# Optimization experiments

Measured on AMD Instinct MI355X. Metric: run time of the kernel, lower is better.

The kernel has to match this reference:

```python
import jax, jax.numpy as jnp
import numpy as np

D = 1024
H = 16
FF = 4 * D


def layer_norm(x, g, b, eps=1e-5):
    mu = jnp.mean(x, axis=-1, keepdims=True)
    var = jnp.var(x, axis=-1, keepdims=True)
    return (x - mu) * jax.lax.rsqrt(var + eps) * g + b


def setup_inputs() -> dict:
    key = jax.random.key(0)
    ks = jax.random.split(key, 8)
    s = lambda fan_in: 1.0 / np.sqrt(fan_in)
    return {
        "x": jax.random.normal(ks[0], (2, 2048, D), dtype=jnp.float32),
        "ln1_g": jnp.ones((D,), jnp.float32),
        "ln1_b": jnp.zeros((D,), jnp.float32),
        "w_qkv": jax.random.uniform(ks[1], (D, 3 * D), jnp.float32, -s(D), s(D)),
        "b_qkv": jnp.zeros((3 * D,), jnp.float32),
        "w_out": jax.random.uniform(ks[2], (D, D), jnp.float32, -s(D), s(D)),
        "b_out": jnp.zeros((D,), jnp.float32),
        "ln2_g": jnp.ones((D,), jnp.float32),
        "ln2_b": jnp.zeros((D,), jnp.float32),
        "w_fc1": jax.random.uniform(ks[3], (D, FF), jnp.float32, -s(D), s(D)),
        "b_fc1": jnp.zeros((FF,), jnp.float32),
        "w_fc2": jax.random.uniform(ks[4], (FF, D), jnp.float32, -s(FF), s(FF)),
        "b_fc2": jnp.zeros((D,), jnp.float32),
    }


def reference(x, ln1_g, ln1_b, w_qkv, b_qkv, w_out, b_out,
              ln2_g, ln2_b, w_fc1, b_fc1, w_fc2, b_fc2):
    b, n, c = x.shape
    hd = c // H
    scale = hd ** -0.5

    # --- pre-norm MHA ---
    h = layer_norm(x, ln1_g, ln1_b)
    qkv = h @ w_qkv + b_qkv                      # [b,n,3c]
    qkv = qkv.reshape(b, n, 3, H, hd)
    q = jnp.transpose(qkv[:, :, 0], (0, 2, 1, 3))  # [b,H,n,hd]
    k = jnp.transpose(qkv[:, :, 1], (0, 2, 1, 3))
    v = jnp.transpose(qkv[:, :, 2], (0, 2, 1, 3))
    attn = jnp.einsum('bhqd,bhkd->bhqk', q, k) * scale
    attn = jax.nn.softmax(attn, axis=-1)
    o = jnp.einsum('bhqk,bhkd->bhqd', attn, v)   # [b,H,n,hd]
    o = jnp.transpose(o, (0, 2, 1, 3)).reshape(b, n, c)
    x = x + (o @ w_out + b_out)

    # --- pre-norm FFN ---
    h = layer_norm(x, ln2_g, ln2_b)
    h = jax.nn.gelu(h @ w_fc1 + b_fc1, approximate=False)
    x = x + (h @ w_fc2 + b_fc2)
    return x
```

## Files before the change

kernel.cpp:

```cpp
#include <hip/hip_runtime.h>
#include <stdint.h>
#include <math.h>

#define D_MODEL 1024
#define NHEAD   16
#define HDIM    64
#define FFDIM   4096
#define SEQ     2048
#define BATCH   2
#define NTOK    (BATCH*SEQ)
#define QKVN    (3*D_MODEL)

typedef __bf16 bf16;
typedef __attribute__((ext_vector_type(8))) __bf16 bf16x8;
typedef __attribute__((ext_vector_type(4))) __bf16 bf16x4;
typedef __attribute__((ext_vector_type(4))) float f32x4;

__device__ __forceinline__ void gld_lds16(const void* g, void* l) {
    __builtin_amdgcn_global_load_lds((__attribute__((address_space(1))) void*)g,
                                     (__attribute__((address_space(3))) void*)l,
                                     16, 0, 0);
}

__device__ __forceinline__ float fast_exp2(float x) {
#if __has_builtin(__builtin_amdgcn_exp2f)
    return __builtin_amdgcn_exp2f(x);
#else
    return __expf(x * 0.69314718056f);
#endif
}

__device__ __forceinline__ float fast_rcp(float x) {
#if __has_builtin(__builtin_amdgcn_rcpf)
    return __builtin_amdgcn_rcpf(x);
#else
    return 1.0f / x;
#endif
}

__device__ __forceinline__ float gelu_fast(float x) {
    float xx = x * x;
    float y  = x * fmaf(0.035677408137f, xx, 0.7978845608f);
    float z  = fminf(-2.8853900817779268f * y, 126.0f);
    float e  = fast_exp2(z);
    return x * fast_rcp(1.0f + e);
}

#define BARRIER() do {                                         \
    __builtin_amdgcn_s_barrier();                              \
    asm volatile("" ::: "memory");                             \
} while (0)
#define LGKM0() asm volatile("s_waitcnt lgkmcnt(0)" ::: "memory")
#define VMW(N)  asm volatile("s_waitcnt vmcnt(" #N ")" ::: "memory")

#define PHASE_BAR() do {                                       \
    asm volatile("s_waitcnt vmcnt(0)" ::: "memory");           \
    __builtin_amdgcn_s_barrier();                              \
    asm volatile("" ::: "memory");                             \
} while (0)

#define GEMM_BAR() do {                                        \
    asm volatile("s_waitcnt lgkmcnt(0)" ::: "memory");         \
    __builtin_amdgcn_s_barrier();                              \
    asm volatile("" ::: "memory");                             \
} while (0)

__global__ __launch_bounds__(256)
void k_transpose_all(const float* __restrict__ w_qkv, const float* __restrict__ w_out,
                     const float* __restrict__ w_fc1, const float* __restrict__ w_fc2,
                     bf16* __restrict__ t_qkv, bf16* __restrict__ t_out,
                     bf16* __restrict__ t_fc1, bf16* __restrict__ t_fc2) {
    __shared__ float tile[32][33];
    int bid = blockIdx.x;
    const float* W; bf16* Wt; int K, N, ti;
    if (bid < 3072)       { W = w_qkv; Wt = t_qkv; K = 1024; N = 3072; ti = bid; }
    else if (bid < 4096)  { W = w_out; Wt = t_out; K = 1024; N = 1024; ti = bid - 3072; }
    else if (bid < 8192)  { W = w_fc1; Wt = t_fc1; K = 1024; N = 4096; ti = bid - 4096; }
    else                  { W = w_fc2; Wt = t_fc2; K = 4096; N = 1024; ti = bid - 8192; }
    int tn = N >> 5;
    int n0 = (ti % tn) * 32, k0 = (ti / tn) * 32;
    int tx = threadIdx.x, ty = threadIdx.y;
#pragma unroll
    for (int i = 0; i < 4; i++)
        tile[ty + i * 8][tx] = W[(size_t)(k0 + ty + i * 8) * N + n0 + tx];
    __syncthreads();
#pragma unroll
    for (int i = 0; i < 4; i++)
        Wt[(size_t)(n0 + ty + i * 8) * K + k0 + tx] = (bf16)tile[tx][ty + i * 8];
}

__global__ __launch_bounds__(256)
void k_vtrans(const bf16* __restrict__ qkv, bf16* __restrict__ vT) {
    __shared__ bf16 t[32][33];
    int tok0 = blockIdx.x * 32, f0 = blockIdx.y * 32;
    int tx = threadIdx.x, ty = threadIdx.y;
#pragma unroll
    for (int i = 0; i < 4; i++)
        t[ty + i * 8][tx] = qkv[(size_t)(tok0 + ty + i * 8) * QKVN + 2 * D_MODEL + f0 + tx];
    __syncthreads();
    int s = tx;
    int pp = (s < 16) ? ((s >> 2) * 8 + (s & 3))
                      : (((s - 16) >> 2) * 8 + ((s - 16) & 3) + 4);
#pragma unroll
    for (int i = 0; i < 4; i++)
        vT[(size_t)(f0 + ty + i * 8) * NTOK + tok0 + pp] = t[tx][ty + i * 8];
}

__global__ __launch_bounds__(256)
void k_layernorm(const float* __restrict__ x, const float* __restrict__ g,
                 const float* __restrict__ b, bf16* __restrict__ out) {
    int row = blockIdx.x;
    int tid = threadIdx.x;
    float4 v = ((const float4*)(x + (size_t)row * D_MODEL))[tid];
    float s  = v.x + v.y + v.z + v.w;
    float ss = v.x * v.x + v.y * v.y + v.z * v.z + v.w * v.w;
#pragma unroll
    for (int off = 32; off > 0; off >>= 1) {
        s  += __shfl_down(s, off, 64);
        ss += __shfl_down(ss, off, 64);
    }
    __shared__ float red[2][4];
    __shared__ float mv[2];
    int wave = tid >> 6, lane = tid & 63;
    if (lane == 0) { red[0][wave] = s; red[1][wave] = ss; }
    __syncthreads();
    if (tid == 0) {
        float S  = red[0][0] + red[0][1] + red[0][2] + red[0][3];
        float SS = red[1][0] + red[1][1] + red[1][2] + red[1][3];
        float mu = S * (1.0f / D_MODEL);
        float var = SS * (1.0f / D_MODEL) - mu * mu;
        mv[0] = mu;
        mv[1] = rsqrtf(var + 1e-5f);
    }
    __syncthreads();
    float mu = mv[0], rs = mv[1];
    float4 gv = ((const float4*)g)[tid];
    float4 bv = ((const float4*)b)[tid];
    bf16x4 ov = { (bf16)((v.x - mu) * rs * gv.x + bv.x),
                  (bf16)((v.y - mu) * rs * gv.y + bv.y),
                  (bf16)((v.z - mu) * rs * gv.z + bv.z),
                  (bf16)((v.w - mu) * rs * gv.w + bv.w) };
    *(bf16x4*)(out + (size_t)row * D_MODEL + tid * 4) = ov;
}

template <int DO_GELU, int ATOMIC, int SPLITK>
__global__ __launch_bounds__(512, 2)
void k_gemm256(const bf16* __restrict__ A, const bf16* __restrict__ Bt,
               const float* __restrict__ bias, bf16* __restrict__ outb,
               float* __restrict__ outf, int M, int N, int K) {
    __shared__ bf16 LA[2][2][8192];
    __shared__ bf16 LB[2][2][8192];

    int tid = threadIdx.x;
    int wid = tid >> 6, lane = tid & 63;
    int quad = lane >> 4, l16 = lane & 15;
    int wm = (wid >> 2) * 128;
    int wn = (wid & 3) * 64;

    int nwg = gridDim.x * gridDim.y;
    int bid = blockIdx.y * gridDim.x + blockIdx.x;
    int sid = (bid & 7) * (nwg >> 3) + (bid >> 3);
    int bx = sid % gridDim.x, by = sid / gridDim.x;
    int m0 = by * 256, n0 = bx * 256;

    int Keff = (SPLITK > 1) ? (K / SPLITK) : K;
    int koff = (SPLITK > 1) ? blockIdx.z * Keff : 0;

    int l = lane;
    int rsw = l >> 2;
    int csw = 8 * ((l & 3) ^ ((l >> 3) & 3));
    const bf16* pA = A  + (size_t)(m0 + 32 * wid + rsw) * K + koff + csw;
    const bf16* pB = Bt + (size_t)(n0 + 32 * wid + rsw) * K + koff + csw;
    int sbase = wid * 1024;

    int xq = 8 * (quad ^ ((l16 >> 1) & 3));

    f32x4 acc[8][4];
#pragma unroll
    for (int i = 0; i < 8; i++)
#pragma unroll
        for (int j = 0; j < 4; j++) acc[i][j] = (f32x4){0.f, 0.f, 0.f, 0.f};

#define STAGE_A(buf, kh, t) do {                                               \
    gld_lds16(pA + (size_t)(t) * 64 + (kh) * 32,              &LA[buf][kh][sbase]);       \
    gld_lds16(pA + (size_t)16 * K + (size_t)(t) * 64 + (kh) * 32, &LA[buf][kh][sbase + 512]); \
} while (0)
#define STAGE_B(buf, kh, t) do {                                               \
    gld_lds16(pB + (size_t)(t) * 64 + (kh) * 32,              &LB[buf][kh][sbase]);       \
    gld_lds16(pB + (size_t)16 * K + (size_t)(t) * 64 + (kh) * 32, &LB[buf][kh][sbase + 512]); \
} while (0)

    bf16x8 af[4], bfr[4];
#define RD_B(buf, kh)  do {                                                    \
    _Pragma("unroll")                                                          \
    for (int fc = 0; fc < 4; fc++)                                             \
        bfr[fc] = *(const bf16x8*)&LB[buf][kh][(wn + fc * 16 + l16) * 32 + xq];\
} while (0)
#define RD_A(buf, kh, rh) do {                                                 \
    _Pragma("unroll")                                                          \
    for (int fr = 0; fr < 4; fr++)                                             \
        af[fr] = *(const bf16x8*)&LA[buf][kh][(wm + (rh) * 64 + fr * 16 + l16) * 32 + xq]; \
} while (0)
#define MFMA16(rh) do {                                                        \
    __builtin_amdgcn_s_setprio(1);                                             \
    _Pragma("unroll")                                                          \
    for (int fr = 0; fr < 4; fr++)                                             \
        _Pragma("unroll")                                                      \
        for (int fc = 0; fc < 4; fc++)                                         \
            acc[(rh) * 4 + fr][fc] =                                           \
                __builtin_amdgcn_mfma_f32_16x16x32_bf16(af[fr], bfr[fc],       \
                                                        acc[(rh) * 4 + fr][fc], 0, 0, 0); \
    __builtin_amdgcn_s_setprio(0);                                             \
} while (0)

    int nt = Keff / 64;
    int buf = 0;
    STAGE_A(0, 0, 0); STAGE_B(0, 0, 0);
    STAGE_A(0, 1, 0); STAGE_B(0, 1, 0);
    VMW(4); BARRIER();

    for (int t = 0; t < nt - 1; t++) {
        RD_B(buf, 0); RD_A(buf, 0, 0);
        STAGE_A(buf ^ 1, 0, t + 1);
        BARRIER(); LGKM0();
        MFMA16(0);
        BARRIER();
        RD_A(buf, 0, 1);
        STAGE_B(buf ^ 1, 0, t + 1);
        BARRIER(); LGKM0();
        MFMA16(1);
        VMW(4); BARRIER();
        RD_B(buf, 1); RD_A(buf, 1, 0);
        STAGE_A(buf ^ 1, 1, t + 1);
        BARRIER(); LGKM0();
        MFMA16(0);
        BARRIER();
        RD_A(buf, 1, 1);
        STAGE_B(buf ^ 1, 1, t + 1);
        BARRIER(); LGKM0();
        MFMA16(1);
        VMW(4); BARRIER();
        buf ^= 1;
    }
    RD_B(buf, 0); RD_A(buf, 0, 0);
    BARRIER(); LGKM0();
    MFMA16(0);
    BARRIER();
    RD_A(buf, 0, 1);
    BARRIER(); LGKM0();
    MFMA16(1);
    VMW(0); BARRIER();
    RD_B(buf, 1); RD_A(buf, 1, 0);
    BARRIER(); LGKM0();
    MFMA16(0);
    BARRIER();
    RD_A(buf, 1, 1);
    LGKM0();
    MFMA16(1);

#undef STAGE_A
#undef STAGE_B
#undef RD_A
#undef RD_B
#undef MFMA16

#pragma unroll
    for (int fi = 0; fi < 8; fi++) {
        int row = m0 + wm + fi * 16 + quad * 4;
#pragma unroll
        for (int fc = 0; fc < 4; fc++) {
            int col = n0 + wn + fc * 16 + l16;
            if constexpr (ATOMIC) {
                float bb = (SPLITK == 1 || blockIdx.z == 0) ? bias[col] : 0.0f;
#pragma unroll
                for (int r = 0; r < 4; r++)
                    atomicAdd(&outf[(size_t)(row + r) * N + col], acc[fi][fc][r] + bb);
            } else {
                float bb = bias[col];
#pragma unroll
                for (int r = 0; r < 4; r++) {
                    float v = acc[fi][fc][r] + bb;
                    if (DO_GELU) v = gelu_fast(v);
                    outb[(size_t)(row + r) * N + col] = (bf16)v;
                }
            }
        }
    }
}

template <int DO_GELU, int DO_RES, int OUT_BF16, int BN>
__global__ __launch_bounds__(256)
void k_gemm(const bf16* __restrict__ A, const bf16* __restrict__ Bt,
            const float* __restrict__ bias, const float* __restrict__ res,
            float* __restrict__ outf, bf16* __restrict__ outb,
            int M, int N, int K) {
    constexpr int WN = BN / 32;
    __shared__ bf16 As[2][128 * 32];
    __shared__ bf16 Bs[2][BN * 32];
    int tid  = threadIdx.x;
    int wave = tid >> 6, lane = tid & 63;
    int quad = lane >> 4, l16 = lane & 15;

    int nwg = gridDim.x * gridDim.y;
    int bid = blockIdx.y * gridDim.x + blockIdx.x;
    int sid = (bid & 7) * (nwg >> 3) + (bid >> 3);
    int bx = sid % gridDim.x, by = sid / gridDim.x;
    int m0 = by * 128, n0 = bx * BN;
    int wm = (wave >> 1) * 64, wn = (wave & 1) * (BN / 2);

    f32x4 acc[4][WN];
#pragma unroll
    for (int i = 0; i < 4; i++)
#pragma unroll
        for (int j = 0; j < WN; j++) acc[i][j] = (f32x4){0.f, 0.f, 0.f, 0.f};

    int lrow = lane >> 2;
    int lcol = (lane & 3) * 8;
    const bf16* gA0 = A + (size_t)(m0 + wave * 32 + lrow) * K + lcol;
    const bf16* gA1 = gA0 + (size_t)16 * K;
    const bf16* gB0;
    const bf16* gB1 = nullptr;
    if constexpr (BN == 128) {
        gB0 = Bt + (size_t)(n0 + wave * 32 + lrow) * K + lcol;
        gB1 = gB0 + (size_t)16 * K;
    } else {
        gB0 = Bt + (size_t)(n0 + wave * 16 + lrow) * K + lcol;
    }

    int wA0 = wave * 1024 + lane * 8;
    int wA1 = wA0 + 512;
    int wB0 = (BN == 128) ? (wave * 1024 + lane * 8) : (wave * 512 + lane * 8);
    int wB1 = wB0 + 512;

    auto issue = [&](bf16x8* r, int k0) {
        r[0] = *(const bf16x8*)(gA0 + k0);
        r[1] = *(const bf16x8*)(gA1 + k0);
        r[2] = *(const bf16x8*)(gB0 + k0);
        if constexpr (BN == 128) r[3] = *(const bf16x8*)(gB1 + k0);
    };
    auto commit = [&](int buf, const bf16x8* r) {
        *(bf16x8*)(&As[buf][wA0]) = r[0];
        *(bf16x8*)(&As[buf][wA1]) = r[1];
        *(bf16x8*)(&Bs[buf][wB0]) = r[2];
        if constexpr (BN == 128) *(bf16x8*)(&Bs[buf][wB1]) = r[3];
    };
    auto compute = [&](const bf16* cA, const bf16* cB) {
        bf16x8 af[4], bfr[WN];
#pragma unroll
        for (int mi = 0; mi < 4; mi++)
            af[mi] = *(const bf16x8*)(cA + (wm + mi * 16 + l16) * 32 + quad * 8);
#pragma unroll
        for (int ni = 0; ni < WN; ni++)
            bfr[ni] = *(const bf16x8*)(cB + (wn + ni * 16 + l16) * 32 + quad * 8);
#pragma unroll
        for (int mi = 0; mi < 4; mi++)
#pragma unroll
            for (int ni = 0; ni < WN; ni++)
                acc[mi][ni] = __builtin_amdgcn_mfma_f32_16x16x32_bf16(af[mi], bfr[ni], acc[mi][ni], 0, 0, 0);
    };

    int niter = K / 32;
    bf16x8 r0[4], r1[4];
    issue(r0, 0);
    commit(0, r0);
    issue(r1, 32);
    GEMM_BAR();
    for (int t = 1; t + 2 < niter; t += 2) {
        issue(r0, (t + 1) * 32);
        compute(&As[0][0], &Bs[0][0]);
        commit(1, r1);
        GEMM_BAR();
        issue(r1, (t + 2) * 32);
        compute(&As[1][0], &Bs[1][0]);
        commit(0, r0);
        GEMM_BAR();
    }
    compute(&As[0][0], &Bs[0][0]);
    commit(1, r1);
    GEMM_BAR();
    compute(&As[1][0], &Bs[1][0]);

#pragma unroll
    for (int mi = 0; mi < 4; mi++) {
        int row = m0 + wm + mi * 16 + quad * 4;
#pragma unroll
        for (int ni = 0; ni < WN; ni++) {
            int col = n0 + wn + ni * 16 + l16;
            float bb = bias[col];
#pragma unroll
            for (int r = 0; r < 4; r++) {
                float v = acc[mi][ni][r] + bb;
                if (DO_GELU) v = gelu_fast(v);
                size_t idx = (size_t)(row + r) * N + col;
                if (DO_RES) v += res[idx];
                if (OUT_BF16) outb[idx] = (bf16)v;
                else          outf[idx] = v;
            }
        }
    }
}

__global__ __launch_bounds__(256)
void k_attention2(const bf16* __restrict__ qkv, const bf16* __restrict__ vT,
                  bf16* __restrict__ o) {
    __shared__ bf16 Ks[2][2][64][32];
    __shared__ bf16 Vs[2][2][64][32];

    int tid = threadIdx.x, wave = tid >> 6, lane = tid & 63;
    int quad = lane >> 4, l16 = lane & 15;
    int bh = blockIdx.y;
    int b = bh >> 4, h = bh & 15;
    int q0 = blockIdx.x * 64 + wave * 16;

    const bf16* Qb  = qkv + (size_t)b * SEQ * QKVN + h * HDIM;
    const bf16* Kb  = Qb + D_MODEL;
    const bf16* vTb = vT + (size_t)h * HDIM * NTOK + b * SEQ;

    const float QSCALE = 0.125f * 1.44269504089f;
    bf16x8 qf[2];
#pragma unroll
    for (int c = 0; c < 2; c++) {
        bf16x8 qraw = *(const bf16x8*)(Qb + (size_t)(q0 + l16) * QKVN + c * 32 + quad * 8);
#pragma unroll
        for (int i = 0; i < 8; i++) qf[c][i] = (bf16)((float)qraw[i] * QSCALE);
    }

    const bf16* gK0 = Kb + (size_t)(wave * 16 + (lane >> 2)) * QKVN + (lane & 3) * 8;
    const bf16* gK1 = gK0 + 32;
    const bf16* gV0 = vTb + (size_t)(wave * 16 + (lane >> 2)) * NTOK + (lane & 3) * 8;
    const bf16* gV1 = gV0 + 32;

    f32x4 oacc[4];
#pragma unroll
    for (int i = 0; i < 4; i++) oacc[i] = (f32x4){0.f, 0.f, 0.f, 0.f};
    float lsum = 0.f;

    gld_lds16(gK0, &Ks[0][0][wave * 16][0]);
    gld_lds16(gK1, &Ks[0][1][wave * 16][0]);
    gld_lds16(gV0, &Vs[0][0][wave * 16][0]);
    gld_lds16(gV1, &Vs[0][1][wave * 16][0]);
    PHASE_BAR();

    int buf = 0;
    for (int kv0 = 0; kv0 < SEQ; kv0 += 64) {
        if (kv0 + 64 < SEQ) {
            size_t koff = (size_t)(kv0 + 64) * QKVN;
            gld_lds16(gK0 + koff, &Ks[buf ^ 1][0][wave * 16][0]);
            gld_lds16(gK1 + koff, &Ks[buf ^ 1][1][wave * 16][0]);
            gld_lds16(gV0 + kv0 + 64, &Vs[buf ^ 1][0][wave * 16][0]);
            gld_lds16(gV1 + kv0 + 64, &Vs[buf ^ 1][1][wave * 16][0]);
        }

        f32x4 s[4];
#pragma unroll
        for (int t = 0; t < 4; t++) {
            bf16x8 af0 = *(const bf16x8*)(&Ks[buf][0][t * 16 + l16][quad * 8]);
            bf16x8 af1 = *(const bf16x8*)(&Ks[buf][1][t * 16 + l16][quad * 8]);
            f32x4 z = (f32x4){0.f, 0.f, 0.f, 0.f};
            z = __builtin_amdgcn_mfma_f32_16x16x32_bf16(af0, qf[0], z, 0, 0, 0);
            z = __builtin_amdgcn_mfma_f32_16x16x32_bf16(af1, qf[1], z, 0, 0, 0);
            s[t] = z;
        }

        bf16x4 p[4];
#pragma unroll
        for (int t = 0; t < 4; t++)
#pragma unroll
            for (int r = 0; r < 4; r++) {
                float pf = fast_exp2(s[t][r]);
                lsum += pf;
                p[t][r] = (bf16)pf;
            }

#pragma unroll
        for (int tp = 0; tp < 2; tp++) {
            bf16x8 pa = __builtin_shufflevector(p[2 * tp], p[2 * tp + 1], 0, 1, 2, 3, 4, 5, 6, 7);
#pragma unroll
            for (int nt = 0; nt < 4; nt++) {
                bf16x8 vb = *(const bf16x8*)(&Vs[buf][tp][nt * 16 + l16][quad * 8]);
                oacc[nt] = __builtin_amdgcn_mfma_f32_16x16x32_bf16(pa, vb, oacc[nt], 0, 0, 0);
            }
        }

        PHASE_BAR();
        buf ^= 1;
    }

    lsum += __shfl_xor(lsum, 16, 64);
    lsum += __shfl_xor(lsum, 32, 64);
    float invl[4];
#pragma unroll
    for (int r = 0; r < 4; r++)
        invl[r] = 1.0f / __shfl(lsum, quad * 4 + r, 16);

#pragma unroll
    for (int nt = 0; nt < 4; nt++)
#pragma unroll
        for (int r = 0; r < 4; r++)
            o[(size_t)(b * SEQ + q0 + quad * 4 + r) * D_MODEL + h * HDIM + nt * 16 + l16] =
                (bf16)(oacc[nt][r] * invl[r]);
}

extern "C" void kernel_launch(void* const* d_in, const int* in_sizes, int n_in,
                              void* d_out, int out_size, void* d_ws, size_t ws_size,
                              hipStream_t stream) {
    const float* x     = (const float*)d_in[0];
    const float* ln1_g = (const float*)d_in[1];
    const float* ln1_b = (const float*)d_in[2];
    const float* w_qkv = (const float*)d_in[3];
    const float* b_qkv = (const float*)d_in[4];
    const float* w_out = (const float*)d_in[5];
    const float* b_out = (const float*)d_in[6];
    const float* ln2_g = (const float*)d_in[7];
    const float* ln2_b = (const float*)d_in[8];
    const float* w_fc1 = (const float*)d_in[9];
    const float* b_fc1 = (const float*)d_in[10];
    const float* w_fc2 = (const float*)d_in[11];
    const float* b_fc2 = (const float*)d_in[12];
    float* out = (float*)d_out;

    uintptr_t ws = (uintptr_t)d_ws;
    bf16* wt_qkv = (bf16*)(ws + 0);
    bf16* wt_out = (bf16*)(ws + 6291456);
    bf16* wt_fc1 = (bf16*)(ws + 8388608);
    bf16* wt_fc2 = (bf16*)(ws + 16777216);
    bf16* hbuf   = (bf16*)(ws + 25165824);
    bf16* vT     = hbuf;
    bf16* qkv    = (bf16*)(ws + 33554432);
    bf16* attn_o = (bf16*)(ws + 58720256);
    bf16* hgelu  = (bf16*)(ws + 33554432);

    k_transpose_all<<<12288, dim3(32, 8), 0, stream>>>(w_qkv, w_out, w_fc1, w_fc2,
                                                       wt_qkv, wt_out, wt_fc1, wt_fc2);

    k_layernorm<<<NTOK, 256, 0, stream>>>(x, ln1_g, ln1_b, hbuf);

    k_gemm256<0, 0, 1><<<dim3(QKVN / 256, NTOK / 256), 512, 0, stream>>>(
        hbuf, wt_qkv, b_qkv, qkv, nullptr, NTOK, QKVN, D_MODEL);

    k_vtrans<<<dim3(NTOK / 32, D_MODEL / 32), dim3(32, 8), 0, stream>>>(qkv, vT);

    k_attention2<<<dim3(SEQ / 64, BATCH * NHEAD), 256, 0, stream>>>(qkv, vT, attn_o);

    k_gemm<0, 1, 0, 64><<<dim3(D_MODEL / 64, NTOK / 128), 256, 0, stream>>>(
        attn_o, wt_out, b_out, x, out, nullptr, NTOK, D_MODEL, D_MODEL);

    k_layernorm<<<NTOK, 256, 0, stream>>>(out, ln2_g, ln2_b, hbuf);

    k_gemm256<1, 0, 1><<<dim3(FFDIM / 256, NTOK / 256), 512, 0, stream>>>(
        hbuf, wt_fc1, b_fc1, hgelu, nullptr, NTOK, FFDIM, D_MODEL);

    k_gemm256<0, 1, 4><<<dim3(D_MODEL / 256, NTOK / 256, 4), 512, 0, stream>>>(
        hgelu, wt_fc2, b_fc2, nullptr, out, NTOK, D_MODEL, FFDIM);
}
```

Before: 359.6 us.

## Deepen gemm256 prefetch pipeline and move FC2 to split-K=2 128-tile GEMM

The 256x256 GEMM now prefetches further ahead. Each K-half of the next tile stages as soon as its buffer is free, and the first half of the tile two steps ahead loads into the current buffer, so up to 8 loads stay in flight instead of 4. The FC2 projection moves off gemm256 with split-K=4 onto the smaller 128x128 k_gemm, which gains a split-K=2 atomic epilogue. This gives more workgroups and halves the number of atomic adds per output. The risk is that the slower k_gemm inner loop costs more on the large-K FC2 than the atomics saved.

```diff
diff --git a/kernel.cpp b/kernel.cpp
--- a/kernel.cpp
+++ b/kernel.cpp
@@ -143,11 +143,11 @@
     *(bf16x4*)(out + (size_t)row * D_MODEL + tid * 4) = ov;
 }
 
-template <int DO_GELU, int ATOMIC, int SPLITK>
+template <int DO_GELU>
 __global__ __launch_bounds__(512, 2)
 void k_gemm256(const bf16* __restrict__ A, const bf16* __restrict__ Bt,
                const float* __restrict__ bias, bf16* __restrict__ outb,
-               float* __restrict__ outf, int M, int N, int K) {
+               int M, int N, int K) {
     __shared__ bf16 LA[2][2][8192];
     __shared__ bf16 LB[2][2][8192];
 
@@ -163,14 +163,11 @@
     int bx = sid % gridDim.x, by = sid / gridDim.x;
     int m0 = by * 256, n0 = bx * 256;
 
-    int Keff = (SPLITK > 1) ? (K / SPLITK) : K;
-    int koff = (SPLITK > 1) ? blockIdx.z * Keff : 0;
-
     int l = lane;
     int rsw = l >> 2;
     int csw = 8 * ((l & 3) ^ ((l >> 3) & 3));
-    const bf16* pA = A  + (size_t)(m0 + 32 * wid + rsw) * K + koff + csw;
-    const bf16* pB = Bt + (size_t)(n0 + 32 * wid + rsw) * K + koff + csw;
+    const bf16* pA = A  + (size_t)(m0 + 32 * wid + rsw) * K + csw;
+    const bf16* pB = Bt + (size_t)(n0 + 32 * wid + rsw) * K + csw;
     int sbase = wid * 1024;
 
     int xq = 8 * (quad ^ ((l16 >> 1) & 3));
@@ -213,33 +210,35 @@
     __builtin_amdgcn_s_setprio(0);                                             \
 } while (0)
 
-    int nt = Keff / 64;
+    int nt = K / 64;
     int buf = 0;
     STAGE_A(0, 0, 0); STAGE_B(0, 0, 0);
     STAGE_A(0, 1, 0); STAGE_B(0, 1, 0);
-    VMW(4); BARRIER();
+    STAGE_A(1, 0, 1); STAGE_B(1, 0, 1);
+    VMW(8); BARRIER();
 
     for (int t = 0; t < nt - 1; t++) {
+        int ts = (t + 2 < nt) ? (t + 2) : (nt - 1);
         RD_B(buf, 0); RD_A(buf, 0, 0);
-        STAGE_A(buf ^ 1, 0, t + 1);
+        STAGE_A(buf ^ 1, 1, t + 1);
         BARRIER(); LGKM0();
         MFMA16(0);
         BARRIER();
         RD_A(buf, 0, 1);
-        STAGE_B(buf ^ 1, 0, t + 1);
+        STAGE_B(buf ^ 1, 1, t + 1);
         BARRIER(); LGKM0();
         MFMA16(1);
-        VMW(4); BARRIER();
+        VMW(8); BARRIER();
         RD_B(buf, 1); RD_A(buf, 1, 0);
-        STAGE_A(buf ^ 1, 1, t + 1);
+        STAGE_A(buf, 0, ts);
         BARRIER(); LGKM0();
         MFMA16(0);
         BARRIER();
         RD_A(buf, 1, 1);
-        STAGE_B(buf ^ 1, 1, t + 1);
+        STAGE_B(buf, 0, ts);
         BARRIER(); LGKM0();
         MFMA16(1);
-        VMW(4); BARRIER();
+        VMW(8); BARRIER();
         buf ^= 1;
     }
     RD_B(buf, 0); RD_A(buf, 0, 0);
@@ -249,7 +248,7 @@
     RD_A(buf, 0, 1);
     BARRIER(); LGKM0();
     MFMA16(1);
-    VMW(0); BARRIER();
+    VMW(4); BARRIER();
     RD_B(buf, 1); RD_A(buf, 1, 0);
     BARRIER(); LGKM0();
     MFMA16(0);
@@ -257,6 +256,7 @@
     RD_A(buf, 1, 1);
     LGKM0();
     MFMA16(1);
+    VMW(0);
 
 #undef STAGE_A
 #undef STAGE_B
@@ -270,25 +270,18 @@
 #pragma unroll
         for (int fc = 0; fc < 4; fc++) {
             int col = n0 + wn + fc * 16 + l16;
-            if constexpr (ATOMIC) {
-                float bb = (SPLITK == 1 || blockIdx.z == 0) ? bias[col] : 0.0f;
-#pragma unroll
-                for (int r = 0; r < 4; r++)
-                    atomicAdd(&outf[(size_t)(row + r) * N + col], acc[fi][fc][r] + bb);
-            } else {
-                float bb = bias[col];
-#pragma unroll
-                for (int r = 0; r < 4; r++) {
-                    float v = acc[fi][fc][r] + bb;
-                    if (DO_GELU) v = gelu_fast(v);
-                    outb[(size_t)(row + r) * N + col] = (bf16)v;
-                }
+            float bb = bias[col];
+#pragma unroll
+            for (int r = 0; r < 4; r++) {
+                float v = acc[fi][fc][r] + bb;
+                if (DO_GELU) v = gelu_fast(v);
+                outb[(size_t)(row + r) * N + col] = (bf16)v;
             }
         }
     }
 }
 
-template <int DO_GELU, int DO_RES, int OUT_BF16, int BN>
+template <int DO_GELU, int DO_RES, int OUT_BF16, int BN, int SPLITK>
 __global__ __launch_bounds__(256)
 void k_gemm(const bf16* __restrict__ A, const bf16* __restrict__ Bt,
             const float* __restrict__ bias, const float* __restrict__ res,
@@ -308,6 +301,9 @@
     int m0 = by * 128, n0 = bx * BN;
     int wm = (wave >> 1) * 64, wn = (wave & 1) * (BN / 2);
 
+    int Keff = (SPLITK == 2) ? (K >> 1) : K;
+    int koff = (SPLITK == 2) ? blockIdx.z * Keff : 0;
+
     f32x4 acc[4][WN];
 #pragma unroll
     for (int i = 0; i < 4; i++)
@@ -316,15 +312,15 @@
 
     int lrow = lane >> 2;
     int lcol = (lane & 3) * 8;
-    const bf16* gA0 = A + (size_t)(m0 + wave * 32 + lrow) * K + lcol;
+    const bf16* gA0 = A + (size_t)(m0 + wave * 32 + lrow) * K + koff + lcol;
     const bf16* gA1 = gA0 + (size_t)16 * K;
     const bf16* gB0;
     const bf16* gB1 = nullptr;
     if constexpr (BN == 128) {
-        gB0 = Bt + (size_t)(n0 + wave * 32 + lrow) * K + lcol;
+        gB0 = Bt + (size_t)(n0 + wave * 32 + lrow) * K + koff + lcol;
         gB1 = gB0 + (size_t)16 * K;
     } else {
-        gB0 = Bt + (size_t)(n0 + wave * 16 + lrow) * K + lcol;
+        gB0 = Bt + (size_t)(n0 + wave * 16 + lrow) * K + koff + lcol;
     }
 
     int wA0 = wave * 1024 + lane * 8;
@@ -359,7 +355,7 @@
                 acc[mi][ni] = __builtin_amdgcn_mfma_f32_16x16x32_bf16(af[mi], bfr[ni], acc[mi][ni], 0, 0, 0);
     };
 
-    int niter = K / 32;
+    int niter = Keff / 32;
     bf16x8 r0[4], r1[4];
     issue(r0, 0);
     commit(0, r0);
@@ -386,6 +382,13 @@
 #pragma unroll
         for (int ni = 0; ni < WN; ni++) {
             int col = n0 + wn + ni * 16 + l16;
+            if constexpr (SPLITK == 2) {
+                float bb = (blockIdx.z == 0) ? bias[col] : 0.0f;
+#pragma unroll
+                for (int r = 0; r < 4; r++)
+                    atomicAdd(&outf[(size_t)(row + r) * N + col], acc[mi][ni][r] + bb);
+                continue;
+            }
             float bb = bias[col];
 #pragma unroll
             for (int r = 0; r < 4; r++) {
@@ -535,21 +538,21 @@
 
     k_layernorm<<<NTOK, 256, 0, stream>>>(x, ln1_g, ln1_b, hbuf);
 
-    k_gemm256<0, 0, 1><<<dim3(QKVN / 256, NTOK / 256), 512, 0, stream>>>(
-        hbuf, wt_qkv, b_qkv, qkv, nullptr, NTOK, QKVN, D_MODEL);
+    k_gemm256<0><<<dim3(QKVN / 256, NTOK / 256), 512, 0, stream>>>(
+        hbuf, wt_qkv, b_qkv, qkv, NTOK, QKVN, D_MODEL);
 
     k_vtrans<<<dim3(NTOK / 32, D_MODEL / 32), dim3(32, 8), 0, stream>>>(qkv, vT);
 
     k_attention2<<<dim3(SEQ / 64, BATCH * NHEAD), 256, 0, stream>>>(qkv, vT, attn_o);
 
-    k_gemm<0, 1, 0, 64><<<dim3(D_MODEL / 64, NTOK / 128), 256, 0, stream>>>(
+    k_gemm<0, 1, 0, 64, 1><<<dim3(D_MODEL / 64, NTOK / 128), 256, 0, stream>>>(
         attn_o, wt_out, b_out, x, out, nullptr, NTOK, D_MODEL, D_MODEL);
 
     k_layernorm<<<NTOK, 256, 0, stream>>>(out, ln2_g, ln2_b, hbuf);
 
-    k_gemm256<1, 0, 1><<<dim3(FFDIM / 256, NTOK / 256), 512, 0, stream>>>(
-        hbuf, wt_fc1, b_fc1, hgelu, nullptr, NTOK, FFDIM, D_MODEL);
-
-    k_gemm256<0, 1, 4><<<dim3(D_MODEL / 256, NTOK / 256, 4), 512, 0, stream>>>(
-        hgelu, wt_fc2, b_fc2, nullptr, out, NTOK, D_MODEL, FFDIM);
-}
+    k_gemm256<1><<<dim3(FFDIM / 256, NTOK / 256), 512, 0, stream>>>(
+        hbuf, wt_fc1, b_fc1, hgelu, NTOK, FFDIM, D_MODEL);
+
+    k_gemm<0, 0, 0, 128, 2><<<dim3(D_MODEL / 128, NTOK / 128, 2), 256, 0, stream>>>(
+        hgelu, wt_fc2, b_fc2, nullptr, out, nullptr, NTOK, D_MODEL, FFDIM);
+}
```

Result: faster. 346.8 us (-3.6%).
